# Performance work log

Measured on AMD Instinct MI355X. Metric: run time of the kernel, lower is better.

The kernel has to match this reference:

```python
import jax, jax.numpy as jnp
import numpy as np

VOCAB, EMB, HID, BATCH, SEQ = 50000, 100, 1024, 256, 512

def _xavier(key, shape):
    fan_in, fan_out = shape[0], shape[1]
    limit = float(np.sqrt(6.0 / (fan_in + fan_out)))
    return jax.random.uniform(key, shape, jnp.float32, -limit, limit)

def setup_inputs() -> dict:
    key = jax.random.key(0)
    ks = jax.random.split(key, 16)
    inp = {
        "tokens": jax.random.randint(ks[0], (BATCH, SEQ), 0, VOCAB),
        "H0": jnp.zeros((BATCH, HID), jnp.float32),
        "C0": jnp.zeros((BATCH, HID), jnp.float32),
        "W_xi": _xavier(ks[1], (EMB, HID)), "W_hi": _xavier(ks[2], (HID, HID)), "b_i": jnp.zeros((HID,), jnp.float32),
        "W_xf": _xavier(ks[3], (EMB, HID)), "W_hf": _xavier(ks[4], (HID, HID)), "b_f": jnp.zeros((HID,), jnp.float32),
        "W_xo": _xavier(ks[5], (EMB, HID)), "W_ho": _xavier(ks[6], (HID, HID)), "b_o": jnp.zeros((HID,), jnp.float32),
        "W_xc": _xavier(ks[7], (EMB, HID)), "W_hc": _xavier(ks[8], (HID, HID)), "b_c": jnp.zeros((HID,), jnp.float32),
        "emb": jax.random.normal(ks[9], (VOCAB, EMB), jnp.float32) * 0.1,
        "dense_w": _xavier(ks[10], (HID, 2)),
        "dense_b": jnp.zeros((2,), jnp.float32),
    }
    return inp

def reference(tokens, H0, C0, W_xi, W_hi, b_i, W_xf, W_hf, b_f,
              W_xo, W_ho, b_o, W_xc, W_hc, b_c, emb, dense_w, dense_b):
    # Embed: [B,S] -> [B,S,E] -> time-major [S,B,E]
    X_seq = jnp.transpose(emb[tokens], (1, 0, 2))
    # Precompute input projections for all timesteps (concatenated-gate GEMM)
    W_x = jnp.concatenate([W_xi, W_xf, W_xo, W_xc], axis=1)   # [E, 4H]
    W_h = jnp.concatenate([W_hi, W_hf, W_ho, W_hc], axis=1)   # [H, 4H]
    b = jnp.concatenate([b_i, b_f, b_o, b_c])                  # [4H]
    XW = jnp.einsum('sbe,eg->sbg', X_seq, W_x) + b             # [S,B,4H]

    def step(carry, xw):
        H, C = carry
        gates = xw + H @ W_h                                   # [B,4H]
        i, f, o, c = jnp.split(gates, 4, axis=-1)
        I = jax.nn.sigmoid(i)
        F = jax.nn.sigmoid(f)
        O = jax.nn.sigmoid(o)
        C_tilda = jnp.tanh(c)
        C = F * C + I * C_tilda
        H = O * jnp.tanh(C)
        return (H, C), None

    (H, C), _ = jax.lax.scan(step, (H0, C0), XW)
    return H @ dense_w + dense_b
```

## Files before the change

### kernel.cpp

```cpp
#include <hip/hip_runtime.h>

typedef _Float16 f16;
typedef _Float16 f16x8 __attribute__((ext_vector_type(8)));
typedef float f32x4 __attribute__((ext_vector_type(4)));

#define STEPS 512
#define BATCHN 256
#define HID 1024
#define EMBN 100
#define KTOT 1152
#define XPAD 128
#define NBLK 256
#define HSLOT ((size_t)BATCHN*HID)

__device__ __forceinline__ float sigm(float x){ return 1.f/(1.f+__expf(-x)); }
__device__ __forceinline__ float tanh_f(float x){
    float e = __expf(2.f*fabsf(x));
    float r = 1.f - 2.f/(e+1.f);
    return x >= 0.f ? r : -r;
}
__device__ __forceinline__ float pick4(float a0, float a1, float a2, float a3, int idx){
    float t0 = (idx & 1) ? a1 : a0;
    float t1 = (idx & 1) ? a3 : a2;
    return (idx & 2) ? t1 : t0;
}

__global__ void pack_w(const float* __restrict__ Whi_, const float* __restrict__ Whf_,
                       const float* __restrict__ Who_, const float* __restrict__ Whc_,
                       const float* __restrict__ Wxi_, const float* __restrict__ Wxf_,
                       const float* __restrict__ Wxo_, const float* __restrict__ Wxc_,
                       const float* __restrict__ bi_, const float* __restrict__ bf_,
                       const float* __restrict__ bo_, const float* __restrict__ bc_,
                       f16* __restrict__ WThi, float* __restrict__ biasP)
{
    int J = blockIdx.x;
    int cg = J >> 6, ct = (J >> 4) & 3, g = (J >> 2) & 3, um = J & 3;
    int u = cg*16 + ct*4 + um;
    const float* Wh = (g==0)?Whi_:(g==1)?Whf_:(g==2)?Who_:Whc_;
    const float* Wx = (g==0)?Wxi_:(g==1)?Wxf_:(g==2)?Wxo_:Wxc_;
    for (int k = threadIdx.x; k < KTOT; k += blockDim.x){
        float v = 0.f;
        if (k < 1024)       v = Wh[(size_t)k*HID + u];
        else if (k < 1124)  v = Wx[(size_t)(k-1024)*HID + u];
        WThi[(size_t)J*KTOT + k] = (f16)v;
    }
    if (threadIdx.x == 0){
        const float* bb = (g==0)?bi_:(g==1)?bf_:(g==2)?bo_:bc_;
        biasP[J] = bb[u];
    }
}

__global__ void pack_x(const int* __restrict__ tokens, const float* __restrict__ emb,
                       f16* __restrict__ Xbuf)
{
    int bid = blockIdx.x;
    int t = bid >> 8, row = bid & 255;
    int tok = tokens[(size_t)row*STEPS + t];
    int kx = threadIdx.x;
    float v = (kx < EMBN) ? emb[(size_t)tok*EMBN + kx] : 0.f;
    Xbuf[(size_t)bid*XPAD + kx] = (f16)v;
}

__global__ void pack_h0(const float* __restrict__ H0, f16* __restrict__ Hb)
{
    int i = blockIdx.x*blockDim.x + threadIdx.x;
    if (i < BATCHN*HID){
        int row = i >> 10, col = i & 1023;
        size_t d = (size_t)(row >> 6)*65536 + (size_t)(col >> 4)*1024
                 + (size_t)(row & 63)*16 + (col & 15);
        Hb[d] = (f16)H0[i];
    }
}

#define ISSUE(kt_, AF) do {                                                              \
    const int kb_ = w*288 + (kt_)*32;                                                    \
    if (kb_ < 1024) {                                                                    \
        const f16* hb_ = Hrd + ((kb_ >> 4) + (lhi >> 1))*1024 + (lhi & 1)*8;             \
        asm volatile("global_load_dwordx4 %0, %1, off" : "=v"(AF[0]) : "v"(hb_ + rS[0])); \
        asm volatile("global_load_dwordx4 %0, %1, off" : "=v"(AF[1]) : "v"(hb_ + rS[1])); \
        asm volatile("global_load_dwordx4 %0, %1, off" : "=v"(AF[2]) : "v"(hb_ + rS[2])); \
        asm volatile("global_load_dwordx4 %0, %1, off" : "=v"(AF[3]) : "v"(hb_ + rS[3])); \
    } else {                                                                             \
        const f16* xb_ = Xrow + (kb_ - 1024) + lhi*8;                                    \
        asm volatile("global_load_dwordx4 %0, %1, off" : "=v"(AF[0]) : "v"(xb_ + (size_t)rA[0]*XPAD)); \
        asm volatile("global_load_dwordx4 %0, %1, off" : "=v"(AF[1]) : "v"(xb_ + (size_t)rA[1]*XPAD)); \
        asm volatile("global_load_dwordx4 %0, %1, off" : "=v"(AF[2]) : "v"(xb_ + (size_t)rA[2]*XPAD)); \
        asm volatile("global_load_dwordx4 %0, %1, off" : "=v"(AF[3]) : "v"(xb_ + (size_t)rA[3]*XPAD)); \
    }                                                                                    \
} while(0)

#define WAITN(n_) do {                                                                   \
    asm volatile("s_waitcnt vmcnt(" #n_ ")" ::: "memory");                               \
    __builtin_amdgcn_sched_barrier(0);                                                   \
} while(0)

#define MM(kt_, AF) do {                                                                 \
    _Pragma("unroll")                                                                    \
    for (int q_ = 0; q_ < 4; q_++){                                                      \
        _Pragma("unroll")                                                                \
        for (int ct_ = 0; ct_ < 4; ct_++){                                               \
            acc[q_][ct_] = __builtin_amdgcn_mfma_f32_16x16x32_f16(AF[q_], Bf[kt_][ct_], acc[q_][ct_], 0,0,0); \
        }                                                                                \
    }                                                                                    \
} while(0)

__global__ __launch_bounds__(256, 1) void lstm_main(
    const f16* __restrict__ WThi, const f16* __restrict__ Xbuf,
    const float* __restrict__ biasP, const float* __restrict__ C0,
    f16* __restrict__ H, int smask, int fmask,
    const float* __restrict__ dw, const float* __restrict__ db,
    float* __restrict__ out, unsigned* __restrict__ flags)
{
    __shared__ f32x4 red[4*3*4*64];
    __shared__ f16 hstage[64*16];
    __shared__ int s_bail;

    const int bid = blockIdx.x;
    const int bg = bid & 3, cg = bid >> 2;
    const int tid = threadIdx.x;
    const int w = tid >> 6, l = tid & 63, lr = l & 15, lhi = l >> 4;
    const int um = l & 3, gs = lr >> 2;
    if (tid == 0) s_bail = 0;

    f16x8 Bf[9][4];
    #pragma unroll
    for (int kt = 0; kt < 9; kt++){
        int k0 = w*288 + kt*32 + lhi*8;
        #pragma unroll
        for (int ct = 0; ct < 4; ct++)
            Bf[kt][ct] = *(const f16x8*)(WThi + (size_t)(cg*64 + ct*16 + lr)*KTOT + k0);
    }
    float bs[4][4];
    #pragma unroll
    for (int ct = 0; ct < 4; ct++)
        #pragma unroll
        for (int g = 0; g < 4; g++)
            bs[ct][g] = biasP[cg*64 + ct*16 + g*4 + um];

    int rA[4], rS[4];
    #pragma unroll
    for (int q = 0; q < 4; q++){
        int rloc = ((w + q) & 3)*16 + lr;
        rA[q] = bg*64 + rloc;
        rS[q] = rloc*16;
    }
    const int myrow0 = bg*64 + w*16 + lhi*4;

    float Cr[4][4];
    #pragma unroll
    for (int ct = 0; ct < 4; ct++)
        #pragma unroll
        for (int r = 0; r < 4; r++)
            Cr[ct][r] = C0[(size_t)(myrow0 + r)*HID + cg*16 + ct*4 + um];

    __syncthreads();

    for (int t = 0; t < STEPS; t++){
        if ((t & fmask) == 0){
            __builtin_amdgcn_fence(__ATOMIC_ACQUIRE, "agent");
            __builtin_amdgcn_sched_barrier(0);
        }

        const f16* Hrd = H + (size_t)(t & smask)*HSLOT + (bg << 16);
        f16*       Hwr = H + (size_t)((t + 1) & smask)*HSLOT + (bg << 16) + (cg << 10);
        const f16* Xrow = Xbuf + (size_t)t*BATCHN*XPAD;

        f32x4 acc[4][4];
        #pragma unroll
        for (int q = 0; q < 4; q++)
            #pragma unroll
            for (int ct = 0; ct < 4; ct++) acc[q][ct] = (f32x4){0.f,0.f,0.f,0.f};

        f16x8 A0[4], A1[4], A2[4], A3[4], A4[4], A5[4], A6[4], A7[4], A8[4];
        ISSUE(0, A0); ISSUE(1, A1); ISSUE(2, A2); ISSUE(3, A3); ISSUE(4, A4);
        ISSUE(5, A5); ISSUE(6, A6); ISSUE(7, A7); ISSUE(8, A8);

        WAITN(32); MM(0, A0);
        WAITN(28); MM(1, A1);
        WAITN(24); MM(2, A2);
        WAITN(20); MM(3, A3);
        WAITN(16); MM(4, A4);
        WAITN(12); MM(5, A5);
        WAITN(8);  MM(6, A6);
        WAITN(4);  MM(7, A7);
        WAITN(0);  MM(8, A8);

        #pragma unroll
        for (int q = 1; q < 4; q++){
            int o = (w + q) & 3;
            #pragma unroll
            for (int ct = 0; ct < 4; ct++)
                red[((o*3 + (q-1))*4 + ct)*64 + l] = acc[q][ct];
        }
        __syncthreads();
        #pragma unroll
        for (int q1 = 0; q1 < 3; q1++)
            #pragma unroll
            for (int ct = 0; ct < 4; ct++)
                acc[0][ct] += red[((w*3 + q1)*4 + ct)*64 + l];

        #pragma unroll
        for (int ct = 0; ct < 4; ct++){
            #pragma unroll
            for (int r = 0; r < 4; r++){
                float a0 = acc[0][ct][r];
                float a1 = __shfl_xor(a0, 4, 64);
                float a2 = __shfl_xor(a0, 8, 64);
                float a3 = __shfl_xor(a0, 12, 64);
                float gi = pick4(a0,a1,a2,a3, gs    ) + bs[ct][0];
                float gf = pick4(a0,a1,a2,a3, gs ^ 1) + bs[ct][1];
                float go = pick4(a0,a1,a2,a3, gs ^ 2) + bs[ct][2];
                float gc = pick4(a0,a1,a2,a3, gs ^ 3) + bs[ct][3];
                float I = sigm(gi), F = sigm(gf), O = sigm(go), G = tanh_f(gc);
                float c = F*Cr[ct][r] + I*G;
                Cr[ct][r] = c;
                float h = O*tanh_f(c);
                if (ct == gs)
                    hstage[(w*16 + lhi*4 + r)*16 + lr] = (f16)h;
            }
        }
        __syncthreads();

        {
            uint2 hv2 = *(const uint2*)(hstage + tid*4);
            const f16* dst = Hwr + tid*4;
            asm volatile("global_store_dwordx2 %0, %1, off sc1" :: "v"(dst), "v"(hv2) : "memory");
        }
        asm volatile("s_waitcnt vmcnt(0)" ::: "memory");
        __syncthreads();

        if (tid == 0)
            __hip_atomic_store(&flags[bg*64 + cg], (unsigned)(t+1), __ATOMIC_RELAXED, __HIP_MEMORY_SCOPE_AGENT);
        if (w == 0){
            unsigned tgt = (unsigned)(t+1), guard = 0;
            for (;;){
                unsigned f0 = __hip_atomic_load(&flags[bg*64 + l], __ATOMIC_RELAXED, __HIP_MEMORY_SCOPE_AGENT);
                if (__all(f0 >= tgt)) break;
                if (++guard > 2000000u){ s_bail = 1; break; }
                __builtin_amdgcn_s_sleep(1);
            }
        }
        __syncthreads();
        if (s_bail) break;
    }

    if (cg == 0){
        const f16* Hf = H + (bg << 16);
        int r = tid >> 2, j = (tid >> 1) & 1, half = tid & 1;
        int row = bg*64 + r;
        float s = 0.f;
        for (int v = 0; v < 64; v++){
            int chunk = half*32 + (v >> 1), koff = (v & 1)*8;
            const f16* hp = Hf + chunk*1024 + r*16 + koff;
            f16x8 h8;
            asm volatile("global_load_dwordx4 %0, %1, off sc1" : "=v"(h8) : "v"(hp));
            asm volatile("s_waitcnt vmcnt(0)" ::: "memory");
            #pragma unroll
            for (int e = 0; e < 8; e++)
                s += (float)h8[e] * dw[(size_t)(half*512 + v*8 + e)*2 + j];
        }
        s += __shfl_xor(s, 1, 64);
        if (half == 0) out[(size_t)row*2 + j] = s + db[j];
    }
}

extern "C" void kernel_launch(void* const* d_in, const int* in_sizes, int n_in,
                              void* d_out, int out_size, void* d_ws, size_t ws_size,
                              hipStream_t stream)
{
    const int*   tokens = (const int*)d_in[0];
    const float* H0  = (const float*)d_in[1];
    const float* C0  = (const float*)d_in[2];
    const float* Wxi = (const float*)d_in[3];
    const float* Whi = (const float*)d_in[4];
    const float* bi  = (const float*)d_in[5];
    const float* Wxf = (const float*)d_in[6];
    const float* Whf = (const float*)d_in[7];
    const float* bf  = (const float*)d_in[8];
    const float* Wxo = (const float*)d_in[9];
    const float* Who = (const float*)d_in[10];
    const float* bo  = (const float*)d_in[11];
    const float* Wxc = (const float*)d_in[12];
    const float* Whc = (const float*)d_in[13];
    const float* bc  = (const float*)d_in[14];
    const float* emb = (const float*)d_in[15];
    const float* dw  = (const float*)d_in[16];
    const float* db  = (const float*)d_in[17];
    float* out = (float*)d_out;

    char* ws = (char*)d_ws;
    size_t off = 0;
    auto alloc = [&](size_t bytes){ void* p = ws + off; off += (bytes + 255) & ~(size_t)255; return p; };
    f16* WThi = (f16*)alloc((size_t)4096*KTOT*2);
    f16* Xbuf = (f16*)alloc((size_t)STEPS*BATCHN*XPAD*2);
    float* biasP = (float*)alloc(4096*sizeof(float));
    unsigned* flags = (unsigned*)alloc(NBLK*sizeof(unsigned));

    size_t ringBytes = (size_t)64*HSLOT*2;
    int smask, fmask;
    f16* H;
    if (off + ringBytes <= ws_size){
        H = (f16*)alloc(ringBytes);
        smask = 63; fmask = 63;
    } else {
        H = (f16*)alloc((size_t)2*HSLOT*2);
        smask = 1; fmask = 0;
    }
    if (off > ws_size) return;

    hipMemsetAsync(flags, 0, NBLK*sizeof(unsigned), stream);
    pack_w<<<4096, 256, 0, stream>>>(Whi,Whf,Who,Whc, Wxi,Wxf,Wxo,Wxc, bi,bf,bo,bc,
                                     WThi, biasP);
    pack_x<<<STEPS*BATCHN, 128, 0, stream>>>(tokens, emb, Xbuf);
    pack_h0<<<(BATCHN*HID + 255)/256, 256, 0, stream>>>(H0, H);
    lstm_main<<<NBLK, 256, 0, stream>>>(WThi, Xbuf, biasP, C0, H, smask, fmask,
                                        dw, db, out, flags);
}
```

Baseline: 5.733 ms.

## Split LSTM recurrence across 512 blocks with 8-column tiles and rolling prefetch

Doubles the persistent grid from 256 to 512 blocks. Each block now owns 8 hidden units (32 gate columns) instead of 16, and the packed weight and H layouts are reworked into 8-column chunks. The nine-deep A-fragment preload is replaced with a three-buffer rolling prefetch, and launch bounds now allow two blocks per CU, aiming to spread the per-step GEMM over more CUs and cut register pressure. In exchange, the per-step barrier must poll 128 flags per batch group, and each block does less MFMA work per synchronisation, so barrier overhead grows relative to compute.

```diff
diff --git a/kernel.cpp b/kernel.cpp
--- a/kernel.cpp
+++ b/kernel.cpp
@@ -10,7 +10,7 @@
 #define EMBN 100
 #define KTOT 1152
 #define XPAD 128
-#define NBLK 256
+#define NBLK 512
 #define HSLOT ((size_t)BATCHN*HID)
 
 __device__ __forceinline__ float sigm(float x){ return 1.f/(1.f+__expf(-x)); }
@@ -34,8 +34,8 @@
                        f16* __restrict__ WThi, float* __restrict__ biasP)
 {
     int J = blockIdx.x;
-    int cg = J >> 6, ct = (J >> 4) & 3, g = (J >> 2) & 3, um = J & 3;
-    int u = cg*16 + ct*4 + um;
+    int cg = J >> 5, ct = (J >> 4) & 1, g = (J >> 2) & 3, um = J & 3;
+    int u = cg*8 + ct*4 + um;
     const float* Wh = (g==0)?Whi_:(g==1)?Whf_:(g==2)?Who_:Whc_;
     const float* Wx = (g==0)?Wxi_:(g==1)?Wxf_:(g==2)?Wxo_:Wxc_;
     for (int k = threadIdx.x; k < KTOT; k += blockDim.x){
@@ -66,8 +66,8 @@
     int i = blockIdx.x*blockDim.x + threadIdx.x;
     if (i < BATCHN*HID){
         int row = i >> 10, col = i & 1023;
-        size_t d = (size_t)(row >> 6)*65536 + (size_t)(col >> 4)*1024
-                 + (size_t)(row & 63)*16 + (col & 15);
+        size_t d = (size_t)(row >> 6)*65536 + (size_t)(col >> 3)*512
+                 + (size_t)(row & 63)*8 + (col & 7);
         Hb[d] = (f16)H0[i];
     }
 }
@@ -75,22 +75,24 @@
 #define ISSUE(kt_, AF) do {                                                              \
     const int kb_ = w*288 + (kt_)*32;                                                    \
     if (kb_ < 1024) {                                                                    \
-        const f16* hb_ = Hrd + ((kb_ >> 4) + (lhi >> 1))*1024 + (lhi & 1)*8;             \
+        const f16* hb_ = Hrd + ((kb_ >> 3) + lhi)*512;                                   \
         asm volatile("global_load_dwordx4 %0, %1, off" : "=v"(AF[0]) : "v"(hb_ + rS[0])); \
         asm volatile("global_load_dwordx4 %0, %1, off" : "=v"(AF[1]) : "v"(hb_ + rS[1])); \
         asm volatile("global_load_dwordx4 %0, %1, off" : "=v"(AF[2]) : "v"(hb_ + rS[2])); \
         asm volatile("global_load_dwordx4 %0, %1, off" : "=v"(AF[3]) : "v"(hb_ + rS[3])); \
     } else {                                                                             \
         const f16* xb_ = Xrow + (kb_ - 1024) + lhi*8;                                    \
-        asm volatile("global_load_dwordx4 %0, %1, off" : "=v"(AF[0]) : "v"(xb_ + (size_t)rA[0]*XPAD)); \
-        asm volatile("global_load_dwordx4 %0, %1, off" : "=v"(AF[1]) : "v"(xb_ + (size_t)rA[1]*XPAD)); \
-        asm volatile("global_load_dwordx4 %0, %1, off" : "=v"(AF[2]) : "v"(xb_ + (size_t)rA[2]*XPAD)); \
-        asm volatile("global_load_dwordx4 %0, %1, off" : "=v"(AF[3]) : "v"(xb_ + (size_t)rA[3]*XPAD)); \
+        asm volatile("global_load_dwordx4 %0, %1, off" : "=v"(AF[0]) : "v"(xb_ + rX[0])); \
+        asm volatile("global_load_dwordx4 %0, %1, off" : "=v"(AF[1]) : "v"(xb_ + rX[1])); \
+        asm volatile("global_load_dwordx4 %0, %1, off" : "=v"(AF[2]) : "v"(xb_ + rX[2])); \
+        asm volatile("global_load_dwordx4 %0, %1, off" : "=v"(AF[3]) : "v"(xb_ + rX[3])); \
     }                                                                                    \
 } while(0)
 
-#define WAITN(n_) do {                                                                   \
-    asm volatile("s_waitcnt vmcnt(" #n_ ")" ::: "memory");                               \
+#define WAITK(kt_) do {                                                                  \
+    if ((kt_) < 7)       asm volatile("s_waitcnt vmcnt(8)" ::: "memory");                \
+    else if ((kt_) == 7) asm volatile("s_waitcnt vmcnt(4)" ::: "memory");                \
+    else                 asm volatile("s_waitcnt vmcnt(0)" ::: "memory");                \
     __builtin_amdgcn_sched_barrier(0);                                                   \
 } while(0)
 
@@ -98,60 +100,60 @@
     _Pragma("unroll")                                                                    \
     for (int q_ = 0; q_ < 4; q_++){                                                      \
         _Pragma("unroll")                                                                \
-        for (int ct_ = 0; ct_ < 4; ct_++){                                               \
+        for (int ct_ = 0; ct_ < 2; ct_++){                                               \
             acc[q_][ct_] = __builtin_amdgcn_mfma_f32_16x16x32_f16(AF[q_], Bf[kt_][ct_], acc[q_][ct_], 0,0,0); \
         }                                                                                \
     }                                                                                    \
 } while(0)
 
-__global__ __launch_bounds__(256, 1) void lstm_main(
+__global__ __launch_bounds__(256, 2) void lstm_main(
     const f16* __restrict__ WThi, const f16* __restrict__ Xbuf,
     const float* __restrict__ biasP, const float* __restrict__ C0,
     f16* __restrict__ H, int smask, int fmask,
     const float* __restrict__ dw, const float* __restrict__ db,
     float* __restrict__ out, unsigned* __restrict__ flags)
 {
-    __shared__ f32x4 red[4*3*4*64];
-    __shared__ f16 hstage[64*16];
+    __shared__ f32x4 red[4*3*2*64];
+    __shared__ f16 hstage[64*8];
     __shared__ int s_bail;
 
     const int bid = blockIdx.x;
-    const int bg = bid & 3, cg = bid >> 2;
+    const int bg = (bid >> 7) & 3, cg = bid & 127;
     const int tid = threadIdx.x;
     const int w = tid >> 6, l = tid & 63, lr = l & 15, lhi = l >> 4;
     const int um = l & 3, gs = lr >> 2;
     if (tid == 0) s_bail = 0;
 
-    f16x8 Bf[9][4];
+    f16x8 Bf[9][2];
     #pragma unroll
     for (int kt = 0; kt < 9; kt++){
         int k0 = w*288 + kt*32 + lhi*8;
         #pragma unroll
-        for (int ct = 0; ct < 4; ct++)
-            Bf[kt][ct] = *(const f16x8*)(WThi + (size_t)(cg*64 + ct*16 + lr)*KTOT + k0);
-    }
-    float bs[4][4];
+        for (int ct = 0; ct < 2; ct++)
+            Bf[kt][ct] = *(const f16x8*)(WThi + (size_t)(cg*32 + ct*16 + lr)*KTOT + k0);
+    }
+    float bs[2][4];
     #pragma unroll
-    for (int ct = 0; ct < 4; ct++)
+    for (int ct = 0; ct < 2; ct++)
         #pragma unroll
         for (int g = 0; g < 4; g++)
-            bs[ct][g] = biasP[cg*64 + ct*16 + g*4 + um];
-
-    int rA[4], rS[4];
+            bs[ct][g] = biasP[cg*32 + ct*16 + g*4 + um];
+
+    int rS[4], rX[4];
     #pragma unroll
     for (int q = 0; q < 4; q++){
         int rloc = ((w + q) & 3)*16 + lr;
-        rA[q] = bg*64 + rloc;
-        rS[q] = rloc*16;
+        rS[q] = rloc*8;
+        rX[q] = (bg*64 + rloc)*XPAD;
     }
     const int myrow0 = bg*64 + w*16 + lhi*4;
 
-    float Cr[4][4];
+    float Cr[2][4];
     #pragma unroll
-    for (int ct = 0; ct < 4; ct++)
+    for (int ct = 0; ct < 2; ct++)
         #pragma unroll
         for (int r = 0; r < 4; r++)
-            Cr[ct][r] = C0[(size_t)(myrow0 + r)*HID + cg*16 + ct*4 + um];
+            Cr[ct][r] = C0[(size_t)(myrow0 + r)*HID + cg*8 + ct*4 + um];
 
     __syncthreads();
 
@@ -161,46 +163,49 @@
             __builtin_amdgcn_sched_barrier(0);
         }
 
-        const f16* Hrd = H + (size_t)(t & smask)*HSLOT + (bg << 16);
-        f16*       Hwr = H + (size_t)((t + 1) & smask)*HSLOT + (bg << 16) + (cg << 10);
+        const f16* Hrd = H + (size_t)(t & smask)*HSLOT + bg*65536;
+        f16*       Hwr = H + (size_t)((t + 1) & smask)*HSLOT + bg*65536 + cg*512;
         const f16* Xrow = Xbuf + (size_t)t*BATCHN*XPAD;
 
-        f32x4 acc[4][4];
+        f32x4 acc[4][2];
         #pragma unroll
         for (int q = 0; q < 4; q++)
             #pragma unroll
-            for (int ct = 0; ct < 4; ct++) acc[q][ct] = (f32x4){0.f,0.f,0.f,0.f};
-
-        f16x8 A0[4], A1[4], A2[4], A3[4], A4[4], A5[4], A6[4], A7[4], A8[4];
-        ISSUE(0, A0); ISSUE(1, A1); ISSUE(2, A2); ISSUE(3, A3); ISSUE(4, A4);
-        ISSUE(5, A5); ISSUE(6, A6); ISSUE(7, A7); ISSUE(8, A8);
-
-        WAITN(32); MM(0, A0);
-        WAITN(28); MM(1, A1);
-        WAITN(24); MM(2, A2);
-        WAITN(20); MM(3, A3);
-        WAITN(16); MM(4, A4);
-        WAITN(12); MM(5, A5);
-        WAITN(8);  MM(6, A6);
-        WAITN(4);  MM(7, A7);
-        WAITN(0);  MM(8, A8);
+            for (int ct = 0; ct < 2; ct++) acc[q][ct] = (f32x4){0.f,0.f,0.f,0.f};
+
+        f16x8 Aa[4], Ab[4], Ac[4];
+        ISSUE(0, Aa);
+        ISSUE(1, Ab);
+        #pragma unroll
+        for (int kt = 0; kt < 9; kt++){
+            if ((kt % 3) == 0){
+                if (kt < 7) ISSUE(kt+2, Ac);
+                WAITK(kt); MM(kt, Aa);
+            } else if ((kt % 3) == 1){
+                if (kt < 7) ISSUE(kt+2, Aa);
+                WAITK(kt); MM(kt, Ab);
+            } else {
+                if (kt < 7) ISSUE(kt+2, Ab);
+                WAITK(kt); MM(kt, Ac);
+            }
+        }
 
         #pragma unroll
         for (int q = 1; q < 4; q++){
             int o = (w + q) & 3;
             #pragma unroll
-            for (int ct = 0; ct < 4; ct++)
-                red[((o*3 + (q-1))*4 + ct)*64 + l] = acc[q][ct];
+            for (int ct = 0; ct < 2; ct++)
+                red[((o*3 + (q-1))*2 + ct)*64 + l] = acc[q][ct];
         }
         __syncthreads();
         #pragma unroll
         for (int q1 = 0; q1 < 3; q1++)
             #pragma unroll
-            for (int ct = 0; ct < 4; ct++)
-                acc[0][ct] += red[((w*3 + q1)*4 + ct)*64 + l];
-
-        #pragma unroll
-        for (int ct = 0; ct < 4; ct++){
+            for (int ct = 0; ct < 2; ct++)
+                acc[0][ct] += red[((w*3 + q1)*2 + ct)*64 + l];
+
+        #pragma unroll
+        for (int ct = 0; ct < 2; ct++){
             #pragma unroll
             for (int r = 0; r < 4; r++){
                 float a0 = acc[0][ct][r];
@@ -216,26 +221,27 @@
                 Cr[ct][r] = c;
                 float h = O*tanh_f(c);
                 if (ct == gs)
-                    hstage[(w*16 + lhi*4 + r)*16 + lr] = (f16)h;
+                    hstage[(w*16 + lhi*4 + r)*8 + gs*4 + um] = (f16)h;
             }
         }
         __syncthreads();
 
         {
-            uint2 hv2 = *(const uint2*)(hstage + tid*4);
-            const f16* dst = Hwr + tid*4;
-            asm volatile("global_store_dwordx2 %0, %1, off sc1" :: "v"(dst), "v"(hv2) : "memory");
+            unsigned hv = *(const unsigned*)(hstage + tid*2);
+            const f16* dst = Hwr + tid*2;
+            asm volatile("global_store_dword %0, %1, off sc1" :: "v"(dst), "v"(hv) : "memory");
         }
         asm volatile("s_waitcnt vmcnt(0)" ::: "memory");
         __syncthreads();
 
         if (tid == 0)
-            __hip_atomic_store(&flags[bg*64 + cg], (unsigned)(t+1), __ATOMIC_RELAXED, __HIP_MEMORY_SCOPE_AGENT);
+            __hip_atomic_store(&flags[bg*128 + cg], (unsigned)(t+1), __ATOMIC_RELAXED, __HIP_MEMORY_SCOPE_AGENT);
         if (w == 0){
             unsigned tgt = (unsigned)(t+1), guard = 0;
             for (;;){
-                unsigned f0 = __hip_atomic_load(&flags[bg*64 + l], __ATOMIC_RELAXED, __HIP_MEMORY_SCOPE_AGENT);
-                if (__all(f0 >= tgt)) break;
+                unsigned f0 = __hip_atomic_load(&flags[bg*128 + l     ], __ATOMIC_RELAXED, __HIP_MEMORY_SCOPE_AGENT);
+                unsigned f1 = __hip_atomic_load(&flags[bg*128 + l + 64], __ATOMIC_RELAXED, __HIP_MEMORY_SCOPE_AGENT);
+                if (__all((f0 >= tgt) && (f1 >= tgt))) break;
                 if (++guard > 2000000u){ s_bail = 1; break; }
                 __builtin_amdgcn_s_sleep(1);
             }
@@ -245,22 +251,29 @@
     }
 
     if (cg == 0){
-        const f16* Hf = H + (bg << 16);
-        int r = tid >> 2, j = (tid >> 1) & 1, half = tid & 1;
-        int row = bg*64 + r;
-        float s = 0.f;
-        for (int v = 0; v < 64; v++){
-            int chunk = half*32 + (v >> 1), koff = (v & 1)*8;
-            const f16* hp = Hf + chunk*1024 + r*16 + koff;
+        const f16* Hf = H + bg*65536;
+        int r = tid >> 2, part = tid & 3;
+        float s0 = 0.f, s1 = 0.f;
+        for (int cc = 0; cc < 32; cc++){
+            int c = part*32 + cc;
             f16x8 h8;
+            const f16* hp = Hf + c*512 + r*8;
             asm volatile("global_load_dwordx4 %0, %1, off sc1" : "=v"(h8) : "v"(hp));
             asm volatile("s_waitcnt vmcnt(0)" ::: "memory");
             #pragma unroll
-            for (int e = 0; e < 8; e++)
-                s += (float)h8[e] * dw[(size_t)(half*512 + v*8 + e)*2 + j];
-        }
-        s += __shfl_xor(s, 1, 64);
-        if (half == 0) out[(size_t)row*2 + j] = s + db[j];
+            for (int e = 0; e < 8; e++){
+                float hv = (float)h8[e];
+                s0 += hv * dw[(size_t)(c*8 + e)*2 + 0];
+                s1 += hv * dw[(size_t)(c*8 + e)*2 + 1];
+            }
+        }
+        s0 += __shfl_xor(s0, 1, 64); s0 += __shfl_xor(s0, 2, 64);
+        s1 += __shfl_xor(s1, 1, 64); s1 += __shfl_xor(s1, 2, 64);
+        if (part == 0){
+            int row = bg*64 + r;
+            out[(size_t)row*2 + 0] = s0 + db[0];
+            out[(size_t)row*2 + 1] = s1 + db[1];
+        }
     }
 }
 
```

After: 5.208 ms. 1.1x faster.
